# Performance work log

Hardware: AMD Instinct MI355X
Metric: run time of the kernel (lower is better)

## Reference

```python
import jax, jax.numpy as jnp
import numpy as np

S, B, SD, OD = 10, 256, 16, 8
H = 10 * (SD * SD + OD * OD)        # 3200, gru hidden
OUT1 = 4 * SD * OD                  # 512
IN = 2 * (SD + OD)                  # 48
TEMP = 0.1                          # concrete-dropout temperature


def setup_inputs() -> dict:
    key = jax.random.key(0)
    ks = jax.random.split(key, 24)
    sc = lambda k, sh, s=0.05: jax.random.normal(k, sh, jnp.float32) * s
    return {
        "y_t": sc(ks[0], (B, OD), 1.0),
        "x_filtered_prev": sc(ks[1], (B, SD), 1.0),
        "x_filtered_prev_prev": sc(ks[2], (B, SD), 1.0),
        "y_prev": sc(ks[3], (B, OD), 1.0),
        "delta_x_prev": sc(ks[4], (B, SD), 1.0),
        "h_prev_ensemble": sc(ks[5], (S, B, H)),
        "F_mat": sc(ks[6], (SD, SD), 0.2),
        "H_mat": sc(ks[7], (OD, SD), 0.2),
        "fc_in_w": sc(ks[8], (H, IN)),
        "fc_in_b": jnp.zeros((H,), jnp.float32),
        "W_ih": sc(ks[9], (3 * H, H), 0.01),
        "W_hh": sc(ks[10], (3 * H, H), 0.01),
        "b_ih": jnp.zeros((3 * H,), jnp.float32),
        "b_hh": jnp.zeros((3 * H,), jnp.float32),
        "fc1_w": sc(ks[11], (OUT1, H)),
        "fc1_b": jnp.zeros((OUT1,), jnp.float32),
        "fc2_w": sc(ks[12], (SD * OD, OUT1)),
        "fc2_b": jnp.zeros((SD * OD,), jnp.float32),
        "p_logit1": jnp.array([0.5], jnp.float32),   # sigmoid -> p in (0.5, 0.8) range
        "p_logit2": jnp.array([1.0], jnp.float32),
        "u1": jax.random.uniform(ks[13], (S, B, H), jnp.float32, 1e-4, 1.0 - 1e-4),
        "u2": jax.random.uniform(ks[14], (S, B, OUT1), jnp.float32, 1e-4, 1.0 - 1e-4),
    }


def _concrete_dropout(x, u, p):
    # relaxed Bernoulli drop mask, scaled to keep expectation
    z = jax.nn.sigmoid((jnp.log(p) - jnp.log1p(-p) + jnp.log(u) - jnp.log1p(-u)) / TEMP)
    return x * (1.0 - z) / (1.0 - p)


def reference(y_t, x_filtered_prev, x_filtered_prev_prev, y_prev, delta_x_prev,
              h_prev_ensemble, F_mat, H_mat, fc_in_w, fc_in_b,
              W_ih, W_hh, b_ih, b_hh, fc1_w, fc1_b, fc2_w, fc2_b,
              p_logit1, p_logit2, u1, u2):
    # system model prediction (nonlinear f, linear h), vectorized over batch
    x_predicted = jnp.tanh(x_filtered_prev @ F_mat.T)          # (B, SD)
    y_predicted = x_predicted @ H_mat.T                        # (B, OD)

    residual = y_t - y_predicted
    diff_state = x_filtered_prev - x_filtered_prev_prev
    inp = jnp.concatenate([delta_x_prev, residual, diff_state, y_prev], axis=-1)  # (B, IN)
    a = jax.nn.relu(inp @ fc_in_w.T + fc_in_b)                 # (B, H) shared across ensemble

    p1 = jax.nn.sigmoid(p_logit1[0])
    p2 = jax.nn.sigmoid(p_logit2[0])

    def gru_cell(x, h):
        gx = x @ W_ih.T + b_ih
        gh = h @ W_hh.T + b_hh
        gx_r, gx_z, gx_n = jnp.split(gx, 3, axis=-1)
        gh_r, gh_z, gh_n = jnp.split(gh, 3, axis=-1)
        r = jax.nn.sigmoid(gx_r + gh_r)
        z = jax.nn.sigmoid(gx_z + gh_z)
        n = jnp.tanh(gx_n + r * gh_n)
        return (1.0 - z) * n + z * h

    def sample_fn(h_i, u1_i, u2_i):
        x = _concrete_dropout(a, u1_i, p1)                     # (B, H)
        h_new = gru_cell(x, h_i)                               # (B, H)
        o = jax.nn.relu(h_new @ fc1_w.T + fc1_b)               # (B, OUT1)
        o = _concrete_dropout(o, u2_i, p2)
        K = (o @ fc2_w.T + fc2_b).reshape(B, SD, OD)           # Kalman gain
        correction = jnp.einsum('bso,bo->bs', K, residual)
        return x_predicted + correction, h_new

    xf_ens, h_new_ens = jax.vmap(sample_fn)(h_prev_ensemble, u1, u2)  # (S,B,SD),(S,B,H)

    x_filtered_final = xf_ens.mean(axis=0)                     # (B, SD)
    diff = xf_ens - x_filtered_final                           # (S, B, SD)
    P_filtered_final = jnp.einsum('sbi,sbj->bij', diff, diff) / S

    # concrete-dropout regularizer (identical per ensemble member)
    ent = lambda p: p * jnp.log(p) + (1.0 - p) * jnp.log1p(-p)
    reg = (jnp.sum(fc_in_w ** 2) / (1.0 - p1) + H * ent(p1)
           + jnp.sum(fc1_w ** 2) / (1.0 - p2) + OUT1 * ent(p2))
    raw_regularization = jnp.full((S,), reg)

    return x_filtered_final, P_filtered_final, raw_regularization
```

## Files before the change

kernel.cpp:

```cpp
#include <hip/hip_runtime.h>
#include <hip/hip_bf16.h>
#include <math.h>

#define S_ENS 10
#define B_DIM 256
#define SD 16
#define OD 8
#define H_DIM 3200
#define OUT1 512
#define IN_DIM 48
#define M_ROWS (S_ENS * B_DIM)
#define TEMP_INV 10.0f

typedef unsigned short u16;
typedef __attribute__((ext_vector_type(8))) short short8;
typedef __attribute__((ext_vector_type(4))) short short4v;
typedef __attribute__((ext_vector_type(4))) float floatx4;

__device__ __forceinline__ float sigmoidf_(float x) { return 1.0f / (1.0f + __expf(-x)); }
__device__ __forceinline__ float fast_tanh(float x) {
    x = fminf(fmaxf(x, -15.f), 15.f);
    float e = __expf(2.f * x);
    return (e - 1.f) / (e + 1.f);
}

__device__ __forceinline__ u16 f2bf(float f) {
    union { float f; unsigned u; } v; v.f = f;
    unsigned u = v.u + 0x7fffu + ((v.u >> 16) & 1u);
    return (u16)(u >> 16);
}
__device__ __forceinline__ float bf2f(u16 h) {
    union { unsigned u; float f; } v; v.u = ((unsigned)h) << 16;
    return v.f;
}

__device__ __forceinline__ void gld_lds16(const u16* g, u16* l) {
    __builtin_amdgcn_global_load_lds((const __attribute__((address_space(1))) void*)g,
                                     (__attribute__((address_space(3))) void*)l, 16, 0, 0);
}

__device__ __forceinline__ void kloop128(const u16* __restrict__ A, const u16* __restrict__ B,
                                         int m_base, int n_base, int kiters,
                                         u16* sA, u16* sB, floatx4 (&acc)[4][4]) {
    const int tid = threadIdx.x;
    const int wave = tid >> 6, lane = tid & 63;
    const int r = tid >> 2, c = tid & 3;
    const int swe = (c ^ ((r >> 1) & 3)) << 3;
    const u16* Ag = A + (size_t)(m_base + r) * H_DIM + swe;
    const u16* Bg = B + (size_t)(n_base + r) * H_DIM + swe;
    u16* sA0 = sA + wave * 512;
    u16* sB0 = sB + wave * 512;
    const int frow = lane & 15, fch = lane >> 4;
    const int wrow0 = (wave >> 1) * 64, wcol0 = (wave & 1) * 64;
    int aoff[4], boff[4];
    #pragma unroll
    for (int mi = 0; mi < 4; ++mi) {
        int row = wrow0 + mi * 16 + frow;
        aoff[mi] = row * 32 + ((fch ^ ((row >> 1) & 3)) << 3);
    }
    #pragma unroll
    for (int ni = 0; ni < 4; ++ni) {
        int row = wcol0 + ni * 16 + frow;
        boff[ni] = row * 32 + ((fch ^ ((row >> 1) & 3)) << 3);
    }
    for (int kk = 0; kk < kiters; ++kk) {
        const u16* ga = Ag + kk * 32;
        const u16* gb = Bg + kk * 32;
        __syncthreads();
        gld_lds16(ga, sA0);
        gld_lds16(ga + (size_t)64 * H_DIM, sA0 + 2048);
        gld_lds16(gb, sB0);
        gld_lds16(gb + (size_t)64 * H_DIM, sB0 + 2048);
        __syncthreads();
        short8 af[4], bfr[4];
        #pragma unroll
        for (int mi = 0; mi < 4; ++mi) af[mi] = *(const short8*)(sA + aoff[mi]);
        #pragma unroll
        for (int ni = 0; ni < 4; ++ni) bfr[ni] = *(const short8*)(sB + boff[ni]);
        #pragma unroll
        for (int mi = 0; mi < 4; ++mi)
            #pragma unroll
            for (int ni = 0; ni < 4; ++ni)
                acc[mi][ni] = __builtin_amdgcn_mfma_f32_16x16x32_bf16(af[mi], bfr[ni], acc[mi][ni], 0, 0, 0);
    }
}

__global__ __launch_bounds__(256) void gru_gemm_a(
    const u16* __restrict__ Xbf, const u16* __restrict__ Hpbf,
    const u16* __restrict__ Wih, const u16* __restrict__ Whh,
    const float* __restrict__ b_ih, const float* __restrict__ b_hh,
    u16* __restrict__ Rb, u16* __restrict__ Zb, u16* __restrict__ Gb) {
    __shared__ u16 sA[4096], sB[4096];
    floatx4 acc[4][4];
    #pragma unroll
    for (int i = 0; i < 4; ++i)
        #pragma unroll
        for (int j = 0; j < 4; ++j) acc[i][j] = (floatx4){0.f, 0.f, 0.f, 0.f};
    const int g = blockIdx.z;
    const int bmi = blockIdx.x, nbi = blockIdx.y;
    const int m_base = bmi * 128, nb = nbi * 128;
    const size_t gstride = (size_t)H_DIM * H_DIM;
    u16* outp;
    if (g == 0) {
        kloop128(Xbf, Wih, m_base, nb, 100, sA, sB, acc);
        kloop128(Hpbf, Whh, m_base, nb, 100, sA, sB, acc);
        outp = Rb;
    } else if (g == 1) {
        kloop128(Xbf, Wih + gstride, m_base, nb, 100, sA, sB, acc);
        kloop128(Hpbf, Whh + gstride, m_base, nb, 100, sA, sB, acc);
        outp = Zb;
    } else {
        kloop128(Hpbf, Whh + 2 * gstride, m_base, nb, 100, sA, sB, acc);
        outp = Gb;
    }
    const int lane = threadIdx.x & 63, wave = threadIdx.x >> 6;
    const int wcol0 = (wave & 1) * 64, cc = lane & 15;
    const size_t tbase = (size_t)(nbi * 20 + bmi) * 16384 + wave * 4096 + lane * 4;
    #pragma unroll
    for (int ni = 0; ni < 4; ++ni) {
        int col = nb + wcol0 + ni * 16 + cc;
        float bsum;
        if (g == 0)      bsum = b_ih[col] + b_hh[col];
        else if (g == 1) bsum = b_ih[H_DIM + col] + b_hh[H_DIM + col];
        else             bsum = b_hh[2 * H_DIM + col];
        #pragma unroll
        for (int mi = 0; mi < 4; ++mi) {
            short4v o;
            #pragma unroll
            for (int j = 0; j < 4; ++j) {
                float v = acc[mi][ni][j] + bsum;
                if (g < 2) v = sigmoidf_(v);
                o[j] = (short)f2bf(v);
            }
            *(short4v*)(outp + tbase + (mi * 4 + ni) * 256) = o;
        }
    }
}

__global__ __launch_bounds__(256) void gru_gemm_b(
    const u16* __restrict__ Xbf, const u16* __restrict__ Wih,
    const u16* __restrict__ Rb, const u16* __restrict__ Zb, const u16* __restrict__ Gb,
    const float* __restrict__ b_ih,
    const float* __restrict__ hprev, u16* __restrict__ Hn) {
    __shared__ u16 sA[4096], sB[4096];
    floatx4 acc[4][4];
    #pragma unroll
    for (int i = 0; i < 4; ++i)
        #pragma unroll
        for (int j = 0; j < 4; ++j) acc[i][j] = (floatx4){0.f, 0.f, 0.f, 0.f};
    const int bmi = blockIdx.x, nbi = blockIdx.y;
    const int m_base = bmi * 128, nb = nbi * 128;
    kloop128(Xbf, Wih + (size_t)2 * H_DIM * H_DIM, m_base, nb, 100, sA, sB, acc);
    const int lane = threadIdx.x & 63, wave = threadIdx.x >> 6;
    const int wrow0 = (wave >> 1) * 64, wcol0 = (wave & 1) * 64;
    const int quad = lane >> 4, cc = lane & 15;
    const size_t tbase = (size_t)(nbi * 20 + bmi) * 16384 + wave * 4096 + lane * 4;
    #pragma unroll
    for (int ni = 0; ni < 4; ++ni) {
        int col = nb + wcol0 + ni * 16 + cc;
        float bin_ = b_ih[2 * H_DIM + col];
        #pragma unroll
        for (int mi = 0; mi < 4; ++mi) {
            size_t pidx = tbase + (mi * 4 + ni) * 256;
            short4v rv = *(const short4v*)(Rb + pidx);
            short4v zv = *(const short4v*)(Zb + pidx);
            short4v gv = *(const short4v*)(Gb + pidx);
            int rw = m_base + wrow0 + mi * 16 + quad * 4;
            #pragma unroll
            for (int j = 0; j < 4; ++j) {
                float r = bf2f((u16)rv[j]);
                float z = bf2f((u16)zv[j]);
                float gh = bf2f((u16)gv[j]);
                float n = fast_tanh(acc[mi][ni][j] + bin_ + r * gh);
                size_t idx = (size_t)(rw + j) * H_DIM + col;
                float h = hprev[idx];
                Hn[idx] = f2bf((1.f - z) * n + z * h);
            }
        }
    }
}

__global__ __launch_bounds__(256) void fc1_k(
    const u16* __restrict__ Hn, const u16* __restrict__ Wb,
    const float* __restrict__ bias, const float* __restrict__ u2,
    const float* __restrict__ pl2, float* __restrict__ O) {
    __shared__ u16 sA[4096], sB[2048];
    floatx4 acc[4][2];
    #pragma unroll
    for (int i = 0; i < 4; ++i) { acc[i][0] = (floatx4){0.f,0.f,0.f,0.f}; acc[i][1] = (floatx4){0.f,0.f,0.f,0.f}; }
    const int tid = threadIdx.x;
    const int wave = tid >> 6, lane = tid & 63;
    const int m_base = blockIdx.y * 128, nb = blockIdx.x * 64;
    const int r = tid >> 2, c = tid & 3;
    const int swe = (c ^ ((r >> 1) & 3)) << 3;
    const u16* Ag = Hn + (size_t)(m_base + r) * H_DIM + swe;
    const u16* Bg = Wb + (size_t)(nb + r) * H_DIM + swe;
    u16* sA0 = sA + wave * 512;
    u16* sB0 = sB + wave * 512;
    const int frow = lane & 15, fch = lane >> 4;
    const int wrow0 = (wave >> 1) * 64, wcol0 = (wave & 1) * 32;
    int aoff[4], boff[2];
    #pragma unroll
    for (int mi = 0; mi < 4; ++mi) {
        int row = wrow0 + mi * 16 + frow;
        aoff[mi] = row * 32 + ((fch ^ ((row >> 1) & 3)) << 3);
    }
    #pragma unroll
    for (int ni = 0; ni < 2; ++ni) {
        int row = wcol0 + ni * 16 + frow;
        boff[ni] = row * 32 + ((fch ^ ((row >> 1) & 3)) << 3);
    }
    for (int kk = 0; kk < 100; ++kk) {
        __syncthreads();
        gld_lds16(Ag + kk * 32, sA0);
        gld_lds16(Ag + kk * 32 + (size_t)64 * H_DIM, sA0 + 2048);
        gld_lds16(Bg + kk * 32, sB0);
        __syncthreads();
        short8 af[4], bfr[2];
        #pragma unroll
        for (int mi = 0; mi < 4; ++mi) af[mi] = *(const short8*)(sA + aoff[mi]);
        #pragma unroll
        for (int ni = 0; ni < 2; ++ni) bfr[ni] = *(const short8*)(sB + boff[ni]);
        #pragma unroll
        for (int mi = 0; mi < 4; ++mi)
            #pragma unroll
            for (int ni = 0; ni < 2; ++ni)
                acc[mi][ni] = __builtin_amdgcn_mfma_f32_16x16x32_bf16(af[mi], bfr[ni], acc[mi][ni], 0, 0, 0);
    }
    float p = sigmoidf_(pl2[0]);
    float lp = __logf(p) - log1pf(-p);
    float inv = 1.0f / (1.0f - p);
    const int quad = lane >> 4, cc = lane & 15;
    #pragma unroll
    for (int ni = 0; ni < 2; ++ni) {
        int col = nb + wcol0 + ni * 16 + cc;
        float bcol = bias[col];
        #pragma unroll
        for (int mi = 0; mi < 4; ++mi) {
            int rw = m_base + wrow0 + mi * 16 + quad * 4;
            #pragma unroll
            for (int j = 0; j < 4; ++j) {
                size_t idx = (size_t)(rw + j) * OUT1 + col;
                float v = fmaxf(acc[mi][ni][j] + bcol, 0.f);
                float u = u2[idx];
                float z = sigmoidf_((lp + __logf(u) - log1pf(-u)) * TEMP_INV);
                O[idx] = v * (1.0f - z) * inv;
            }
        }
    }
}

__global__ void cvt_bf16_k(const float* __restrict__ src, u16* __restrict__ dst, int n8) {
    int i = blockIdx.x * 256 + threadIdx.x;
    if (i >= n8) return;
    float4 v0 = *((const float4*)src + 2 * (size_t)i);
    float4 v1 = *((const float4*)src + 2 * (size_t)i + 1);
    short8 o;
    o[0] = (short)f2bf(v0.x); o[1] = (short)f2bf(v0.y);
    o[2] = (short)f2bf(v0.z); o[3] = (short)f2bf(v0.w);
    o[4] = (short)f2bf(v1.x); o[5] = (short)f2bf(v1.y);
    o[6] = (short)f2bf(v1.z); o[7] = (short)f2bf(v1.w);
    *(short8*)(dst + 8 * (size_t)i) = o;
}

__global__ void prep_k(const float* __restrict__ y_t, const float* __restrict__ xfp,
                       const float* __restrict__ xfpp, const float* __restrict__ yprev,
                       const float* __restrict__ dxp, const float* __restrict__ Fm,
                       const float* __restrict__ Hm,
                       float* __restrict__ xpred, float* __restrict__ resid,
                       float* __restrict__ inp) {
    int b = threadIdx.x;
    float xrow[SD], xp[SD];
    for (int k = 0; k < SD; ++k) xrow[k] = xfp[b * SD + k];
    for (int s = 0; s < SD; ++s) {
        float acc = 0.f;
        for (int k = 0; k < SD; ++k) acc += xrow[k] * Fm[s * SD + k];
        xp[s] = tanhf(acc);
        xpred[b * SD + s] = xp[s];
    }
    float res[OD];
    for (int o = 0; o < OD; ++o) {
        float acc = 0.f;
        for (int s = 0; s < SD; ++s) acc += xp[s] * Hm[o * SD + s];
        res[o] = y_t[b * OD + o] - acc;
        resid[b * OD + o] = res[o];
    }
    float* ir = inp + b * IN_DIM;
    for (int k = 0; k < SD; ++k) ir[k] = dxp[b * SD + k];
    for (int o = 0; o < OD; ++o) ir[SD + o] = res[o];
    for (int k = 0; k < SD; ++k) ir[SD + OD + k] = xrow[k] - xfpp[b * SD + k];
    for (int o = 0; o < OD; ++o) ir[SD + OD + SD + o] = yprev[b * OD + o];
}

__global__ void fc_in_k(const float* __restrict__ inp, const float* __restrict__ w,
                        const float* __restrict__ bias, float* __restrict__ a) {
    int b = blockIdx.x;
    __shared__ float row[IN_DIM];
    int t = threadIdx.x;
    if (t < IN_DIM) row[t] = inp[b * IN_DIM + t];
    __syncthreads();
    for (int j = t; j < H_DIM; j += 256) {
        float s = bias[j];
        const float* wr = w + j * IN_DIM;
        #pragma unroll 8
        for (int k = 0; k < IN_DIM; ++k) s += row[k] * wr[k];
        a[b * H_DIM + j] = fmaxf(s, 0.f);
    }
}

__global__ void dropx_k(const float* __restrict__ a, const float* __restrict__ u1,
                        const float* __restrict__ pl1, u16* __restrict__ X) {
    int idx_in = blockIdx.x * 256 + threadIdx.x;
    int i = blockIdx.y;
    float p = sigmoidf_(pl1[0]);
    float lp = __logf(p) - log1pf(-p);
    float inv = 1.0f / (1.0f - p);
    size_t gidx = (size_t)i * (B_DIM * H_DIM) + idx_in;
    float u = u1[gidx];
    float z = sigmoidf_((lp + __logf(u) - log1pf(-u)) * TEMP_INV);
    X[gidx] = f2bf(a[idx_in] * (1.0f - z) * inv);
}

__global__ void fc2_corr_k(const float* __restrict__ O, const float* __restrict__ w,
                           const float* __restrict__ bias, const float* __restrict__ resid,
                           const float* __restrict__ xpred, float* __restrict__ xf_ens) {
    int row = blockIdx.x;
    int b = row & (B_DIM - 1);
    __shared__ __align__(16) float orow[OUT1];
    int t = threadIdx.x;
    for (int k = t; k < OUT1; k += 128) orow[k] = O[(size_t)row * OUT1 + k];
    __syncthreads();
    int s = t >> 3, oo = t & 7;
    const float* wr = w + (s * OD + oo) * OUT1;
    float sum = 0.f;
    for (int k = 0; k < OUT1; k += 4) {
        float4 ov = *(const float4*)&orow[k];
        float4 wv = *(const float4*)&wr[k];
        sum += ov.x * wv.x + ov.y * wv.y + ov.z * wv.z + ov.w * wv.w;
    }
    sum += bias[s * OD + oo];
    float v = sum * resid[b * OD + oo];
    v += __shfl_down(v, 4, 8);
    v += __shfl_down(v, 2, 8);
    v += __shfl_down(v, 1, 8);
    if (oo == 0) xf_ens[row * SD + s] = xpred[b * SD + s] + v;
}

__global__ void stats_k(const float* __restrict__ xf_ens, float* __restrict__ out) {
    int b = blockIdx.x;
    __shared__ float xf[S_ENS][SD];
    __shared__ float mean[SD];
    int t = threadIdx.x;
    if (t < S_ENS * SD) {
        int s = t >> 4, k = t & 15;
        xf[s][k] = xf_ens[s * (B_DIM * SD) + b * SD + k];
    }
    __syncthreads();
    if (t < SD) {
        float m = 0.f;
        for (int s = 0; s < S_ENS; ++s) m += xf[s][t];
        m *= (1.0f / S_ENS);
        mean[t] = m;
        out[b * SD + t] = m;
    }
    __syncthreads();
    int i = t >> 4, j = t & 15;
    float p = 0.f;
    for (int s = 0; s < S_ENS; ++s) p += (xf[s][i] - mean[i]) * (xf[s][j] - mean[j]);
    out[B_DIM * SD + b * 256 + t] = p * (1.0f / S_ENS);
}

__global__ void sumsq_k(const float* __restrict__ w, int n, float* __restrict__ accum) {
    float s = 0.f;
    for (int i = blockIdx.x * blockDim.x + threadIdx.x; i < n; i += gridDim.x * blockDim.x) {
        float v = w[i];
        s += v * v;
    }
    #pragma unroll
    for (int d = 32; d >= 1; d >>= 1) s += __shfl_down(s, d, 64);
    __shared__ float red[4];
    int lane = threadIdx.x & 63, wv = threadIdx.x >> 6;
    if (lane == 0) red[wv] = s;
    __syncthreads();
    if (threadIdx.x == 0) atomicAdd(accum, red[0] + red[1] + red[2] + red[3]);
}

__global__ void write_reg_k(const float* __restrict__ sums, const float* __restrict__ pl1,
                            const float* __restrict__ pl2, float* __restrict__ out) {
    int t = threadIdx.x;
    float p1 = sigmoidf_(pl1[0]);
    float p2 = sigmoidf_(pl2[0]);
    float ent1 = p1 * logf(p1) + (1.f - p1) * log1pf(-p1);
    float ent2 = p2 * logf(p2) + (1.f - p2) * log1pf(-p2);
    float reg = sums[0] / (1.f - p1) + (float)H_DIM * ent1
              + sums[1] / (1.f - p2) + (float)OUT1 * ent2;
    if (t < S_ENS) out[B_DIM * SD + B_DIM * SD * SD + t] = reg;
}

extern "C" void kernel_launch(void* const* d_in, const int* in_sizes, int n_in,
                              void* d_out, int out_size, void* d_ws, size_t ws_size,
                              hipStream_t stream) {
    const float* y_t     = (const float*)d_in[0];
    const float* xfp     = (const float*)d_in[1];
    const float* xfpp    = (const float*)d_in[2];
    const float* yprev   = (const float*)d_in[3];
    const float* dxp     = (const float*)d_in[4];
    const float* hprev   = (const float*)d_in[5];
    const float* Fm      = (const float*)d_in[6];
    const float* Hm      = (const float*)d_in[7];
    const float* fc_in_w = (const float*)d_in[8];
    const float* fc_in_b = (const float*)d_in[9];
    const float* W_ih    = (const float*)d_in[10];
    const float* W_hh    = (const float*)d_in[11];
    const float* b_ih    = (const float*)d_in[12];
    const float* b_hh    = (const float*)d_in[13];
    const float* fc1_w   = (const float*)d_in[14];
    const float* fc1_b   = (const float*)d_in[15];
    const float* fc2_w   = (const float*)d_in[16];
    const float* fc2_b   = (const float*)d_in[17];
    const float* pl1     = (const float*)d_in[18];
    const float* pl2     = (const float*)d_in[19];
    const float* u1      = (const float*)d_in[20];
    const float* u2      = (const float*)d_in[21];
    float* out = (float*)d_out;
    char* ws = (char*)d_ws;

    const size_t SZ_W    = (size_t)3 * H_DIM * H_DIM * 2;
    const size_t SZ_MH   = (size_t)M_ROWS * H_DIM * 2;
    size_t off = 0;
    u16* Wihbf  = (u16*)(ws + off); off += SZ_W;
    u16* Whhbf  = (u16*)(ws + off); off += SZ_W;
    u16* Rb     = (u16*)(ws + off); off += SZ_MH;
    u16* Zb     = (u16*)(ws + off); off += SZ_MH;
    u16* Gb     = (u16*)(ws + off); off += SZ_MH;
    u16* Xbf    = (u16*)(ws + off); off += SZ_MH;
    u16* Hpbf   = (u16*)(ws + off); off += SZ_MH;
    u16* Hnbf   = Hpbf;
    u16* fc1wbf = (u16*)(ws + off); off += (size_t)OUT1 * H_DIM * 2;
    float* O_buf   = (float*)(ws + off); off += (size_t)M_ROWS * OUT1 * 4;
    float* a_buf   = (float*)(ws + off); off += (size_t)B_DIM * H_DIM * 4;
    float* xf_buf  = (float*)(ws + off); off += (size_t)M_ROWS * SD * 4;
    float* xpred_b = (float*)(ws + off); off += (size_t)B_DIM * SD * 4;
    float* res_b   = (float*)(ws + off); off += (size_t)B_DIM * OD * 4;
    float* inp_b   = (float*)(ws + off); off += (size_t)B_DIM * IN_DIM * 4;
    float* sums_b  = (float*)(ws + off); off += 256;

    hipMemsetAsync(sums_b, 0, 2 * sizeof(float), stream);

    prep_k<<<1, 256, 0, stream>>>(y_t, xfp, xfpp, yprev, dxp, Fm, Hm, xpred_b, res_b, inp_b);
    fc_in_k<<<B_DIM, 256, 0, stream>>>(inp_b, fc_in_w, fc_in_b, a_buf);
    dropx_k<<<dim3(B_DIM * H_DIM / 256, S_ENS), 256, 0, stream>>>(a_buf, u1, pl1, Xbf);

    cvt_bf16_k<<<15000, 256, 0, stream>>>(W_ih, Wihbf, 3 * H_DIM * H_DIM / 8);
    cvt_bf16_k<<<15000, 256, 0, stream>>>(W_hh, Whhbf, 3 * H_DIM * H_DIM / 8);
    cvt_bf16_k<<<4000, 256, 0, stream>>>(hprev, Hpbf, M_ROWS * H_DIM / 8);
    cvt_bf16_k<<<800, 256, 0, stream>>>(fc1_w, fc1wbf, OUT1 * H_DIM / 8);

    gru_gemm_a<<<dim3(M_ROWS / 128, H_DIM / 128, 3), 256, 0, stream>>>(
        Xbf, Hpbf, Wihbf, Whhbf, b_ih, b_hh, Rb, Zb, Gb);
    gru_gemm_b<<<dim3(M_ROWS / 128, H_DIM / 128), 256, 0, stream>>>(
        Xbf, Wihbf, Rb, Zb, Gb, b_ih, hprev, Hnbf);

    fc1_k<<<dim3(OUT1 / 64, M_ROWS / 128), 256, 0, stream>>>(Hnbf, fc1wbf, fc1_b, u2, pl2, O_buf);

    fc2_corr_k<<<M_ROWS, 128, 0, stream>>>(O_buf, fc2_w, fc2_b, res_b, xpred_b, xf_buf);
    stats_k<<<B_DIM, 256, 0, stream>>>(xf_buf, out);
    sumsq_k<<<256, 256, 0, stream>>>(fc_in_w, H_DIM * IN_DIM, sums_b);
    sumsq_k<<<1024, 256, 0, stream>>>(fc1_w, OUT1 * H_DIM, sums_b + 1);
    write_reg_k<<<1, 64, 0, stream>>>(sums_b, pl1, pl2, out);
}
```

Measured before the change: 1.009 ms.

## Rewrite GRU GEMMs as 256x128 double-buffered, 8-wave ping-pong pipelined kernels

Result: slower. 1.086 ms (+7.6%).

```diff
diff --git a/kernel.cpp b/kernel.cpp
--- a/kernel.cpp
+++ b/kernel.cpp
@@ -39,146 +39,236 @@
                                      (__attribute__((address_space(3))) void*)l, 16, 0, 0);
 }
 
-__device__ __forceinline__ void kloop128(const u16* __restrict__ A, const u16* __restrict__ B,
-                                         int m_base, int n_base, int kiters,
-                                         u16* sA, u16* sB, floatx4 (&acc)[4][4]) {
+__device__ __forceinline__ void bar_() {
+    __builtin_amdgcn_sched_barrier(0);
+    asm volatile("" ::: "memory");
+    __builtin_amdgcn_s_barrier();
+    asm volatile("" ::: "memory");
+    __builtin_amdgcn_sched_barrier(0);
+}
+#define VMCNT4() asm volatile("s_waitcnt vmcnt(4)" ::: "memory")
+
+#define RDA(BUF, QM) do {                                                          \
+    _Pragma("unroll")                                                              \
+    for (int mi_ = 0; mi_ < 4; ++mi_) {                                            \
+        af[mi_][0] = *(const short8*)(sA + (((BUF)*2 + (QM))*2 + 0)*4096 + aro[mi_]); \
+        af[mi_][1] = *(const short8*)(sA + (((BUF)*2 + (QM))*2 + 1)*4096 + aro[mi_]); \
+    } } while (0)
+
+#define RDB(BUF, QN, BS) do {                                                      \
+    BS[0] = *(const short8*)(sB + (((BUF)*2 + (QN))*2 + 0)*2048 + bro);            \
+    BS[1] = *(const short8*)(sB + (((BUF)*2 + (QN))*2 + 1)*2048 + bro);            \
+    } while (0)
+
+#define MMAQ(QM, QN, BS) do {                                                      \
+    __builtin_amdgcn_s_setprio(1);                                                 \
+    _Pragma("unroll")                                                              \
+    for (int mi_ = 0; mi_ < 4; ++mi_) {                                            \
+        acc[QM][QN][mi_] = __builtin_amdgcn_mfma_f32_16x16x32_bf16(af[mi_][0], BS[0], acc[QM][QN][mi_], 0, 0, 0); \
+        acc[QM][QN][mi_] = __builtin_amdgcn_mfma_f32_16x16x32_bf16(af[mi_][1], BS[1], acc[QM][QN][mi_], 0, 0, 0); \
+    }                                                                              \
+    __builtin_amdgcn_s_setprio(0); } while (0)
+
+__device__ __forceinline__ void kloop8(
+    const u16* __restrict__ A0, const u16* __restrict__ A1,
+    const u16* __restrict__ B0, const u16* __restrict__ B1,
+    int nts, int nt, int m_base, int n_base,
+    u16* sA, u16* sB, floatx4 (&acc)[2][2][4])
+{
     const int tid = threadIdx.x;
-    const int wave = tid >> 6, lane = tid & 63;
-    const int r = tid >> 2, c = tid & 3;
-    const int swe = (c ^ ((r >> 1) & 3)) << 3;
-    const u16* Ag = A + (size_t)(m_base + r) * H_DIM + swe;
-    const u16* Bg = B + (size_t)(n_base + r) * H_DIM + swe;
-    u16* sA0 = sA + wave * 512;
-    u16* sB0 = sB + wave * 512;
-    const int frow = lane & 15, fch = lane >> 4;
-    const int wrow0 = (wave >> 1) * 64, wcol0 = (wave & 1) * 64;
-    int aoff[4], boff[4];
+    const int w = tid >> 6, l = tid & 63;
+    const int wm = w >> 2, wn = w & 3;
+
+    const int rr = l >> 2, c4 = l & 3;
+    const int achn = (c4 ^ ((rr >> 1) & 3)) << 3;
+    const size_t a_off = (size_t)(w * 16 + rr) * H_DIM + achn;
+    const size_t b_off = (size_t)((w & 3) * 16 + rr) * H_DIM + achn;
+    const int bj = w >> 2;
+
+    const int frow = l & 15, fch = l >> 4;
+    int aro[4];
     #pragma unroll
     for (int mi = 0; mi < 4; ++mi) {
-        int row = wrow0 + mi * 16 + frow;
-        aoff[mi] = row * 32 + ((fch ^ ((row >> 1) & 3)) << 3);
-    }
-    #pragma unroll
-    for (int ni = 0; ni < 4; ++ni) {
-        int row = wcol0 + ni * 16 + frow;
-        boff[ni] = row * 32 + ((fch ^ ((row >> 1) & 3)) << 3);
-    }
-    for (int kk = 0; kk < kiters; ++kk) {
-        const u16* ga = Ag + kk * 32;
-        const u16* gb = Bg + kk * 32;
-        __syncthreads();
-        gld_lds16(ga, sA0);
-        gld_lds16(ga + (size_t)64 * H_DIM, sA0 + 2048);
-        gld_lds16(gb, sB0);
-        gld_lds16(gb + (size_t)64 * H_DIM, sB0 + 2048);
-        __syncthreads();
-        short8 af[4], bfr[4];
-        #pragma unroll
-        for (int mi = 0; mi < 4; ++mi) af[mi] = *(const short8*)(sA + aoff[mi]);
-        #pragma unroll
-        for (int ni = 0; ni < 4; ++ni) bfr[ni] = *(const short8*)(sB + boff[ni]);
-        #pragma unroll
-        for (int mi = 0; mi < 4; ++mi)
-            #pragma unroll
-            for (int ni = 0; ni < 4; ++ni)
-                acc[mi][ni] = __builtin_amdgcn_mfma_f32_16x16x32_bf16(af[mi], bfr[ni], acc[mi][ni], 0, 0, 0);
-    }
-}
-
-__global__ __launch_bounds__(256) void gru_gemm_a(
+        int r = wm * 64 + mi * 16 + frow;
+        aro[mi] = r * 32 + ((fch ^ ((r >> 1) & 3)) << 3);
+    }
+    int bro;
+    { int r = wn * 16 + frow; bro = r * 32 + ((fch ^ ((r >> 1) & 3)) << 3); }
+
+    auto stA = [&](int tau, int h) {
+        int tc = tau < nt ? tau : nt - 1;
+        const u16* p = (tc < nts) ? A0 : A1;
+        int k = ((tc < nts) ? tc : tc - nts) << 6;
+        const u16* src = p + (size_t)(m_base + h * 128) * H_DIM + a_off + k;
+        u16* dst = sA + (((tc & 1) * 2 + h) * 2) * 4096 + w * 512;
+        gld_lds16(src, dst);
+        gld_lds16(src + 32, dst + 4096);
+    };
+    auto stB = [&](int tau, int h) {
+        int tc = tau < nt ? tau : nt - 1;
+        const u16* p = (tc < nts) ? B0 : B1;
+        int k = ((tc < nts) ? tc : tc - nts) << 6;
+        const u16* src = p + (size_t)(n_base + h * 64) * H_DIM + b_off + k + bj * 32;
+        u16* dst = sB + (((tc & 1) * 2 + h) * 2 + bj) * 2048 + (w & 3) * 512;
+        gld_lds16(src, dst);
+    };
+
+    stA(0, 0); stB(0, 0); stB(0, 1); stA(0, 1);
+    stA(1, 0); stB(1, 0); stB(1, 1);
+    VMCNT4();
+    bar_();
+
+    short8 af[4][2], bf0[2], bf1[2];
+    const int niter = nt >> 1;
+    for (int i = 0; i < niter; ++i) {
+        const int t = 2 * i;
+        RDA(0, 0); RDB(0, 0, bf0);
+        stA(t + 1, 1);
+        bar_();
+        MMAQ(0, 0, bf0);
+        bar_();
+        RDB(0, 1, bf1);
+        stA(t + 2, 0);
+        bar_();
+        MMAQ(0, 1, bf1);
+        bar_();
+        RDA(0, 1);
+        stB(t + 2, 0);
+        bar_();
+        MMAQ(1, 0, bf0);
+        bar_();
+        stB(t + 2, 1);
+        bar_();
+        MMAQ(1, 1, bf1);
+        VMCNT4();
+        bar_();
+        RDA(1, 0); RDB(1, 0, bf0);
+        stA(t + 2, 1);
+        bar_();
+        MMAQ(0, 0, bf0);
+        bar_();
+        RDB(1, 1, bf1);
+        stA(t + 3, 0);
+        bar_();
+        MMAQ(0, 1, bf1);
+        bar_();
+        RDA(1, 1);
+        stB(t + 3, 0);
+        bar_();
+        MMAQ(1, 0, bf0);
+        bar_();
+        stB(t + 3, 1);
+        bar_();
+        MMAQ(1, 1, bf1);
+        VMCNT4();
+        bar_();
+    }
+}
+
+__global__ __launch_bounds__(512, 2) void gru_gemm_a(
     const u16* __restrict__ Xbf, const u16* __restrict__ Hpbf,
     const u16* __restrict__ Wih, const u16* __restrict__ Whh,
     const float* __restrict__ b_ih, const float* __restrict__ b_hh,
     u16* __restrict__ Rb, u16* __restrict__ Zb, u16* __restrict__ Gb) {
-    __shared__ u16 sA[4096], sB[4096];
-    floatx4 acc[4][4];
-    #pragma unroll
-    for (int i = 0; i < 4; ++i)
-        #pragma unroll
-        for (int j = 0; j < 4; ++j) acc[i][j] = (floatx4){0.f, 0.f, 0.f, 0.f};
+    __shared__ u16 sA[32768];
+    __shared__ u16 sB[16384];
+    floatx4 acc[2][2][4];
+    #pragma unroll
+    for (int a = 0; a < 2; ++a)
+        #pragma unroll
+        for (int b = 0; b < 2; ++b)
+            #pragma unroll
+            for (int c = 0; c < 4; ++c) acc[a][b][c] = (floatx4){0.f, 0.f, 0.f, 0.f};
     const int g = blockIdx.z;
     const int bmi = blockIdx.x, nbi = blockIdx.y;
-    const int m_base = bmi * 128, nb = nbi * 128;
+    const int m_base = bmi * 256, n_base = nbi * 128;
     const size_t gstride = (size_t)H_DIM * H_DIM;
-    u16* outp;
-    if (g == 0) {
-        kloop128(Xbf, Wih, m_base, nb, 100, sA, sB, acc);
-        kloop128(Hpbf, Whh, m_base, nb, 100, sA, sB, acc);
-        outp = Rb;
-    } else if (g == 1) {
-        kloop128(Xbf, Wih + gstride, m_base, nb, 100, sA, sB, acc);
-        kloop128(Hpbf, Whh + gstride, m_base, nb, 100, sA, sB, acc);
-        outp = Zb;
+    if (g < 2) {
+        kloop8(Xbf, Hpbf, Wih + g * gstride, Whh + g * gstride, 50, 100, m_base, n_base, sA, sB, acc);
     } else {
-        kloop128(Hpbf, Whh + 2 * gstride, m_base, nb, 100, sA, sB, acc);
-        outp = Gb;
-    }
-    const int lane = threadIdx.x & 63, wave = threadIdx.x >> 6;
-    const int wcol0 = (wave & 1) * 64, cc = lane & 15;
-    const size_t tbase = (size_t)(nbi * 20 + bmi) * 16384 + wave * 4096 + lane * 4;
-    #pragma unroll
-    for (int ni = 0; ni < 4; ++ni) {
-        int col = nb + wcol0 + ni * 16 + cc;
-        float bsum;
-        if (g == 0)      bsum = b_ih[col] + b_hh[col];
-        else if (g == 1) bsum = b_ih[H_DIM + col] + b_hh[H_DIM + col];
-        else             bsum = b_hh[2 * H_DIM + col];
-        #pragma unroll
-        for (int mi = 0; mi < 4; ++mi) {
-            short4v o;
+        kloop8(Hpbf, Hpbf, Whh + 2 * gstride, Whh + 2 * gstride, 50, 50, m_base, n_base, sA, sB, acc);
+    }
+    u16* outp = (g == 0) ? Rb : (g == 1) ? Zb : Gb;
+    const int tid = threadIdx.x;
+    const int w = tid >> 6, lane = tid & 63;
+    const int wn = w & 3, cc = lane & 15;
+    const size_t tbase = (size_t)(nbi * 10 + bmi) * 32768 + w * 4096 + lane * 4;
+    #pragma unroll
+    for (int qm = 0; qm < 2; ++qm)
+        #pragma unroll
+        for (int qn = 0; qn < 2; ++qn) {
+            int col = n_base + qn * 64 + wn * 16 + cc;
+            float bsum;
+            if (g == 0)      bsum = b_ih[col] + b_hh[col];
+            else if (g == 1) bsum = b_ih[H_DIM + col] + b_hh[H_DIM + col];
+            else             bsum = b_hh[2 * H_DIM + col];
             #pragma unroll
-            for (int j = 0; j < 4; ++j) {
-                float v = acc[mi][ni][j] + bsum;
-                if (g < 2) v = sigmoidf_(v);
-                o[j] = (short)f2bf(v);
+            for (int mi = 0; mi < 4; ++mi) {
+                short4v o;
+                #pragma unroll
+                for (int j = 0; j < 4; ++j) {
+                    float v = acc[qm][qn][mi][j] + bsum;
+                    if (g < 2) v = sigmoidf_(v);
+                    o[j] = (short)f2bf(v);
+                }
+                *(short4v*)(outp + tbase + ((qm * 2 + qn) * 4 + mi) * 256) = o;
             }
-            *(short4v*)(outp + tbase + (mi * 4 + ni) * 256) = o;
         }
-    }
-}
-
-__global__ __launch_bounds__(256) void gru_gemm_b(
+}
+
+__global__ __launch_bounds__(512, 2) void gru_gemm_b(
     const u16* __restrict__ Xbf, const u16* __restrict__ Wih,
     const u16* __restrict__ Rb, const u16* __restrict__ Zb, const u16* __restrict__ Gb,
     const float* __restrict__ b_ih,
     const float* __restrict__ hprev, u16* __restrict__ Hn) {
-    __shared__ u16 sA[4096], sB[4096];
-    floatx4 acc[4][4];
-    #pragma unroll
-    for (int i = 0; i < 4; ++i)
-        #pragma unroll
-        for (int j = 0; j < 4; ++j) acc[i][j] = (floatx4){0.f, 0.f, 0.f, 0.f};
+    __shared__ u16 sA[32768];
+    __shared__ u16 sB[16384];
+    floatx4 acc[2][2][4];
+    #pragma unroll
+    for (int a = 0; a < 2; ++a)
+        #pragma unroll
+        for (int b = 0; b < 2; ++b)
+            #pragma unroll
+            for (int c = 0; c < 4; ++c) acc[a][b][c] = (floatx4){0.f, 0.f, 0.f, 0.f};
     const int bmi = blockIdx.x, nbi = blockIdx.y;
-    const int m_base = bmi * 128, nb = nbi * 128;
-    kloop128(Xbf, Wih + (size_t)2 * H_DIM * H_DIM, m_base, nb, 100, sA, sB, acc);
-    const int lane = threadIdx.x & 63, wave = threadIdx.x >> 6;
-    const int wrow0 = (wave >> 1) * 64, wcol0 = (wave & 1) * 64;
+    const int m_base = bmi * 256, n_base = nbi * 128;
+    const u16* Wn = Wih + (size_t)2 * H_DIM * H_DIM;
+    kloop8(Xbf, Xbf, Wn, Wn, 50, 50, m_base, n_base, sA, sB, acc);
+    const int tid = threadIdx.x;
+    const int w = tid >> 6, lane = tid & 63;
+    const int wm = w >> 2, wn = w & 3;
     const int quad = lane >> 4, cc = lane & 15;
-    const size_t tbase = (size_t)(nbi * 20 + bmi) * 16384 + wave * 4096 + lane * 4;
-    #pragma unroll
-    for (int ni = 0; ni < 4; ++ni) {
-        int col = nb + wcol0 + ni * 16 + cc;
-        float bin_ = b_ih[2 * H_DIM + col];
-        #pragma unroll
-        for (int mi = 0; mi < 4; ++mi) {
-            size_t pidx = tbase + (mi * 4 + ni) * 256;
-            short4v rv = *(const short4v*)(Rb + pidx);
-            short4v zv = *(const short4v*)(Zb + pidx);
-            short4v gv = *(const short4v*)(Gb + pidx);
-            int rw = m_base + wrow0 + mi * 16 + quad * 4;
+    const size_t tbase = (size_t)(nbi * 10 + bmi) * 32768 + w * 4096 + lane * 4;
+    #pragma unroll
+    for (int qm = 0; qm < 2; ++qm)
+        #pragma unroll
+        for (int qn = 0; qn < 2; ++qn) {
+            int col = n_base + qn * 64 + wn * 16 + cc;
+            float bin_ = b_ih[2 * H_DIM + col];
             #pragma unroll
-            for (int j = 0; j < 4; ++j) {
-                float r = bf2f((u16)rv[j]);
-                float z = bf2f((u16)zv[j]);
-                float gh = bf2f((u16)gv[j]);
-                float n = fast_tanh(acc[mi][ni][j] + bin_ + r * gh);
-                size_t idx = (size_t)(rw + j) * H_DIM + col;
-                float h = hprev[idx];
-                Hn[idx] = f2bf((1.f - z) * n + z * h);
+            for (int mi = 0; mi < 4; ++mi) {
+                size_t pidx = tbase + ((qm * 2 + qn) * 4 + mi) * 256;
+                short4v rv = *(const short4v*)(Rb + pidx);
+                short4v zv = *(const short4v*)(Zb + pidx);
+                short4v gv = *(const short4v*)(Gb + pidx);
+                int rw = m_base + qm * 128 + wm * 64 + mi * 16 + quad * 4;
+                #pragma unroll
+                for (int j = 0; j < 4; ++j) {
+                    float r = bf2f((u16)rv[j]);
+                    float z = bf2f((u16)zv[j]);
+                    float gh = bf2f((u16)gv[j]);
+                    float n = fast_tanh(acc[qm][qn][mi][j] + bin_ + r * gh);
+                    size_t idx = (size_t)(rw + j) * H_DIM + col;
+                    float h = hprev[idx];
+                    Hn[idx] = f2bf((1.f - z) * n + z * h);
+                }
             }
         }
-    }
-}
+}
+
+#undef RDA
+#undef RDB
+#undef MMAQ
 
 __global__ __launch_bounds__(256) void fc1_k(
     const u16* __restrict__ Hn, const u16* __restrict__ Wb,
@@ -456,9 +546,9 @@
     cvt_bf16_k<<<4000, 256, 0, stream>>>(hprev, Hpbf, M_ROWS * H_DIM / 8);
     cvt_bf16_k<<<800, 256, 0, stream>>>(fc1_w, fc1wbf, OUT1 * H_DIM / 8);
 
-    gru_gemm_a<<<dim3(M_ROWS / 128, H_DIM / 128, 3), 256, 0, stream>>>(
+    gru_gemm_a<<<dim3(M_ROWS / 256, H_DIM / 128, 3), 512, 0, stream>>>(
         Xbf, Hpbf, Wihbf, Whhbf, b_ih, b_hh, Rb, Zb, Gb);
-    gru_gemm_b<<<dim3(M_ROWS / 128, H_DIM / 128), 256, 0, stream>>>(
+    gru_gemm_b<<<dim3(M_ROWS / 256, H_DIM / 128), 512, 0, stream>>>(
         Xbf, Wihbf, Rb, Zb, Gb, b_ih, hprev, Hnbf);
 
     fc1_k<<<dim3(OUT1 / 64, M_ROWS / 128), 256, 0, stream>>>(Hnbf, fc1wbf, fc1_b, u2, pl2, O_buf);
```

## Double-buffer GEMM K-loop with async LDS prefetch and ping-pong MFMA phases

Applied to the files above, without the earlier changes.

After: 989.5 us. -2.0%, faster.

```diff
diff --git a/kernel.cpp b/kernel.cpp
--- a/kernel.cpp
+++ b/kernel.cpp
@@ -39,17 +39,25 @@
                                      (__attribute__((address_space(3))) void*)l, 16, 0, 0);
 }
 
-__device__ __forceinline__ void kloop128(const u16* __restrict__ A, const u16* __restrict__ B,
-                                         int m_base, int n_base, int kiters,
-                                         u16* sA, u16* sB, floatx4 (&acc)[4][4]) {
+__device__ __forceinline__ void bar_() {
+    __builtin_amdgcn_sched_barrier(0);
+    asm volatile("" ::: "memory");
+    __builtin_amdgcn_s_barrier();
+    asm volatile("" ::: "memory");
+    __builtin_amdgcn_sched_barrier(0);
+}
+#define VMCNT4() asm volatile("s_waitcnt vmcnt(4)" ::: "memory")
+
+__device__ __forceinline__ void kloop128(
+    const u16* __restrict__ A0, const u16* __restrict__ A1,
+    const u16* __restrict__ B0, const u16* __restrict__ B1,
+    int nts, int nt, int m_base, int n_base,
+    u16* sA, u16* sB, floatx4 (&acc)[4][4])
+{
     const int tid = threadIdx.x;
     const int wave = tid >> 6, lane = tid & 63;
     const int r = tid >> 2, c = tid & 3;
     const int swe = (c ^ ((r >> 1) & 3)) << 3;
-    const u16* Ag = A + (size_t)(m_base + r) * H_DIM + swe;
-    const u16* Bg = B + (size_t)(n_base + r) * H_DIM + swe;
-    u16* sA0 = sA + wave * 512;
-    u16* sB0 = sB + wave * 512;
     const int frow = lane & 15, fch = lane >> 4;
     const int wrow0 = (wave >> 1) * 64, wcol0 = (wave & 1) * 64;
     int aoff[4], boff[4];
@@ -63,25 +71,77 @@
         int row = wcol0 + ni * 16 + frow;
         boff[ni] = row * 32 + ((fch ^ ((row >> 1) & 3)) << 3);
     }
-    for (int kk = 0; kk < kiters; ++kk) {
-        const u16* ga = Ag + kk * 32;
-        const u16* gb = Bg + kk * 32;
-        __syncthreads();
-        gld_lds16(ga, sA0);
-        gld_lds16(ga + (size_t)64 * H_DIM, sA0 + 2048);
-        gld_lds16(gb, sB0);
-        gld_lds16(gb + (size_t)64 * H_DIM, sB0 + 2048);
-        __syncthreads();
-        short8 af[4], bfr[4];
-        #pragma unroll
-        for (int mi = 0; mi < 4; ++mi) af[mi] = *(const short8*)(sA + aoff[mi]);
-        #pragma unroll
-        for (int ni = 0; ni < 4; ++ni) bfr[ni] = *(const short8*)(sB + boff[ni]);
+
+    auto stA = [&](int tau) {
+        int tc = tau < nt ? tau : nt - 1;
+        const u16* p = (tc < nts) ? A0 : A1;
+        int k = ((tc < nts) ? tc : tc - nts) << 6;
+        const u16* src = p + (size_t)(m_base + r) * H_DIM + swe + k;
+        u16* dst = sA + (tc & 1) * 8192 + wave * 512;
+        gld_lds16(src, dst);
+        gld_lds16(src + (size_t)64 * H_DIM, dst + 2048);
+        gld_lds16(src + 32, dst + 4096);
+        gld_lds16(src + 32 + (size_t)64 * H_DIM, dst + 6144);
+    };
+    auto stB = [&](int tau) {
+        int tc = tau < nt ? tau : nt - 1;
+        const u16* p = (tc < nts) ? B0 : B1;
+        int k = ((tc < nts) ? tc : tc - nts) << 6;
+        const u16* src = p + (size_t)(n_base + r) * H_DIM + swe + k;
+        u16* dst = sB + (tc & 1) * 8192 + wave * 512;
+        gld_lds16(src, dst);
+        gld_lds16(src + (size_t)64 * H_DIM, dst + 2048);
+        gld_lds16(src + 32, dst + 4096);
+        gld_lds16(src + 32 + (size_t)64 * H_DIM, dst + 6144);
+    };
+
+    stA(0); stB(0); stA(1);
+    VMCNT4();
+    bar_();
+
+    for (int t = 0; t < nt; ++t) {
+        const int bo = (t & 1) * 8192;
+        short8 af[4][2], bfr[4][2];
+        #pragma unroll
+        for (int mi = 0; mi < 4; ++mi) {
+            af[mi][0] = *(const short8*)(sA + bo + aoff[mi]);
+            af[mi][1] = *(const short8*)(sA + bo + 4096 + aoff[mi]);
+        }
+        #pragma unroll
+        for (int ni = 0; ni < 2; ++ni) {
+            bfr[ni][0] = *(const short8*)(sB + bo + boff[ni]);
+            bfr[ni][1] = *(const short8*)(sB + bo + 4096 + boff[ni]);
+        }
+        stB(t + 1);
+        bar_();
+        __builtin_amdgcn_s_setprio(1);
         #pragma unroll
         for (int mi = 0; mi < 4; ++mi)
             #pragma unroll
-            for (int ni = 0; ni < 4; ++ni)
-                acc[mi][ni] = __builtin_amdgcn_mfma_f32_16x16x32_bf16(af[mi], bfr[ni], acc[mi][ni], 0, 0, 0);
+            for (int ni = 0; ni < 2; ++ni) {
+                acc[mi][ni] = __builtin_amdgcn_mfma_f32_16x16x32_bf16(af[mi][0], bfr[ni][0], acc[mi][ni], 0, 0, 0);
+                acc[mi][ni] = __builtin_amdgcn_mfma_f32_16x16x32_bf16(af[mi][1], bfr[ni][1], acc[mi][ni], 0, 0, 0);
+            }
+        __builtin_amdgcn_s_setprio(0);
+        bar_();
+        #pragma unroll
+        for (int ni = 2; ni < 4; ++ni) {
+            bfr[ni][0] = *(const short8*)(sB + bo + boff[ni]);
+            bfr[ni][1] = *(const short8*)(sB + bo + 4096 + boff[ni]);
+        }
+        stA(t + 2);
+        bar_();
+        __builtin_amdgcn_s_setprio(1);
+        #pragma unroll
+        for (int mi = 0; mi < 4; ++mi)
+            #pragma unroll
+            for (int ni = 2; ni < 4; ++ni) {
+                acc[mi][ni] = __builtin_amdgcn_mfma_f32_16x16x32_bf16(af[mi][0], bfr[ni][0], acc[mi][ni], 0, 0, 0);
+                acc[mi][ni] = __builtin_amdgcn_mfma_f32_16x16x32_bf16(af[mi][1], bfr[ni][1], acc[mi][ni], 0, 0, 0);
+            }
+        __builtin_amdgcn_s_setprio(0);
+        VMCNT4();
+        bar_();
     }
 }
 
@@ -90,7 +150,7 @@
     const u16* __restrict__ Wih, const u16* __restrict__ Whh,
     const float* __restrict__ b_ih, const float* __restrict__ b_hh,
     u16* __restrict__ Rb, u16* __restrict__ Zb, u16* __restrict__ Gb) {
-    __shared__ u16 sA[4096], sB[4096];
+    __shared__ u16 sA[16384], sB[16384];
     floatx4 acc[4][4];
     #pragma unroll
     for (int i = 0; i < 4; ++i)
@@ -100,19 +160,12 @@
     const int bmi = blockIdx.x, nbi = blockIdx.y;
     const int m_base = bmi * 128, nb = nbi * 128;
     const size_t gstride = (size_t)H_DIM * H_DIM;
-    u16* outp;
-    if (g == 0) {
-        kloop128(Xbf, Wih, m_base, nb, 100, sA, sB, acc);
-        kloop128(Hpbf, Whh, m_base, nb, 100, sA, sB, acc);
-        outp = Rb;
-    } else if (g == 1) {
-        kloop128(Xbf, Wih + gstride, m_base, nb, 100, sA, sB, acc);
-        kloop128(Hpbf, Whh + gstride, m_base, nb, 100, sA, sB, acc);
-        outp = Zb;
+    if (g < 2) {
+        kloop128(Xbf, Hpbf, Wih + g * gstride, Whh + g * gstride, 50, 100, m_base, nb, sA, sB, acc);
     } else {
-        kloop128(Hpbf, Whh + 2 * gstride, m_base, nb, 100, sA, sB, acc);
-        outp = Gb;
-    }
+        kloop128(Hpbf, Hpbf, Whh + 2 * gstride, Whh + 2 * gstride, 50, 50, m_base, nb, sA, sB, acc);
+    }
+    u16* outp = (g == 0) ? Rb : (g == 1) ? Zb : Gb;
     const int lane = threadIdx.x & 63, wave = threadIdx.x >> 6;
     const int wcol0 = (wave & 1) * 64, cc = lane & 15;
     const size_t tbase = (size_t)(nbi * 20 + bmi) * 16384 + wave * 4096 + lane * 4;
@@ -142,7 +195,7 @@
     const u16* __restrict__ Rb, const u16* __restrict__ Zb, const u16* __restrict__ Gb,
     const float* __restrict__ b_ih,
     const float* __restrict__ hprev, u16* __restrict__ Hn) {
-    __shared__ u16 sA[4096], sB[4096];
+    __shared__ u16 sA[16384], sB[16384];
     floatx4 acc[4][4];
     #pragma unroll
     for (int i = 0; i < 4; ++i)
@@ -150,7 +203,8 @@
         for (int j = 0; j < 4; ++j) acc[i][j] = (floatx4){0.f, 0.f, 0.f, 0.f};
     const int bmi = blockIdx.x, nbi = blockIdx.y;
     const int m_base = bmi * 128, nb = nbi * 128;
-    kloop128(Xbf, Wih + (size_t)2 * H_DIM * H_DIM, m_base, nb, 100, sA, sB, acc);
+    const u16* Wn = Wih + (size_t)2 * H_DIM * H_DIM;
+    kloop128(Xbf, Xbf, Wn, Wn, 50, 50, m_base, nb, sA, sB, acc);
     const int lane = threadIdx.x & 63, wave = threadIdx.x >> 6;
     const int wrow0 = (wave >> 1) * 64, wcol0 = (wave & 1) * 64;
     const int quad = lane >> 4, cc = lane & 15;
```
